# Kernel tuning notes

Hardware: AMD Instinct MI355X
Metric: run time of the kernel (lower is better)

## Reference

```python
import jax, jax.numpy as jnp
import numpy as np


def setup_inputs() -> dict:
    key = jax.random.key(0)
    ks = jax.random.split(key, 6)
    B, T, D, E, F = 2, 2048, 1024, 8, 2048
    x = jax.random.normal(ks[0], (B, T, D), dtype=jnp.float32)
    gate_w = jax.random.normal(ks[1], (D, E), dtype=jnp.float32) * (1.0 / np.sqrt(D))
    base_w1 = jax.random.normal(ks[2], (D, F), dtype=jnp.float32) * np.sqrt(2.0 / (D + F))
    base_w2 = jax.random.normal(ks[3], (F, D), dtype=jnp.float32) * np.sqrt(2.0 / (F + D))
    expert_w1 = base_w1[None] + jax.random.normal(ks[4], (E, D, F), dtype=jnp.float32) * 0.01
    expert_w2 = base_w2[None] + jax.random.normal(ks[5], (E, F, D), dtype=jnp.float32) * 0.01
    expert_b1 = jnp.zeros((E, F), dtype=jnp.float32)
    expert_b2 = jnp.zeros((E, D), dtype=jnp.float32)
    return {"x": x, "gate_w": gate_w, "expert_w1": expert_w1, "expert_b1": expert_b1,
            "expert_w2": expert_w2, "expert_b2": expert_b2}


def reference(x, gate_w, expert_w1, expert_b1, expert_w2, expert_b2):
    # Router (TopKRouter): top-2 routing with aux load-balance loss + z-loss
    E = gate_w.shape[-1]
    TOP_K = 2
    Z_LOSS_COEF = 1e-3
    logits = jnp.einsum('btd,de->bte', x, gate_w)                       # [B,T,E]
    top_vals, top_idx = jax.lax.top_k(logits, TOP_K)                    # [B,T,K]
    router_weights = jax.nn.softmax(top_vals, axis=-1)                  # [B,T,K]
    probs = jax.nn.softmax(logits, axis=-1)
    mask = jax.nn.one_hot(top_idx[..., 0], E, dtype=x.dtype)            # top-1 expert mask
    tokens_per_expert = mask.mean(axis=(0, 1))                          # [E]
    router_prob_per_expert = probs.mean(axis=(0, 1))                    # [E]
    aux_loss = E * jnp.sum(tokens_per_expert * router_prob_per_expert) \
               + jnp.mean(logits ** 2) * Z_LOSS_COEF

    # Expert FFNs: compute all experts densely, then gather top-k outputs.
    # (Same math as per-token weight gather, without the BTDF intermediate.)
    h = jnp.einsum('btd,edf->btef', x, expert_w1) + expert_b1           # [B,T,E,F]
    h = jax.nn.gelu(h, approximate=False)                               # torch F.gelu default = erf
    out_all = jnp.einsum('btef,efd->bted', h, expert_w2) + expert_b2    # [B,T,E,D]
    gathered = jnp.take_along_axis(out_all, top_idx[..., None], axis=2) # [B,T,K,D]
    output = jnp.einsum('btk,btkd->btd', router_weights, gathered)      # [B,T,D]
    return output, aux_loss
```

## Files before the change

kernel.cpp:

```cpp
#include <hip/hip_runtime.h>
#include <hip/hip_bf16.h>

#define NTOK 4096
#define DDIM 1024
#define NEXP 8
#define FDIM 2048
#define CAP  4096
#define RTOK 16
#define MT   16

typedef float f32x4 __attribute__((ext_vector_type(4)));
typedef short s16x8 __attribute__((ext_vector_type(8)));
typedef short s16x4 __attribute__((ext_vector_type(4)));

__device__ __forceinline__ unsigned short f2bf(float f) {
  unsigned int u = __float_as_uint(f);
  unsigned int r = u + 0x7fffu + ((u >> 16) & 1u);
  return (unsigned short)(r >> 16);
}

__device__ __forceinline__ void gload16(const void* g, void* l) {
  __builtin_amdgcn_global_load_lds(
      (__attribute__((address_space(1))) unsigned int*)(g),
      (__attribute__((address_space(3))) unsigned int*)(l), 16, 0, 0);
}

__global__ __launch_bounds__(256)
void k_transpose_cast(const float* __restrict__ src, unsigned short* __restrict__ dst,
                      int R, int C) {
  __shared__ float tile[64][68];
  const int e = blockIdx.z;
  const int c0 = blockIdx.x * 64, r0 = blockIdx.y * 64;
  const float* s = src + (size_t)e * R * C;
  unsigned short* d = dst + (size_t)e * R * C;
  const int tid = threadIdx.x;
  const int lr = tid >> 4, lc = (tid & 15) * 4;
  #pragma unroll
  for (int p = 0; p < 4; p++) {
    float4 v = *(const float4*)(s + (size_t)(r0 + p * 16 + lr) * C + c0 + lc);
    tile[p * 16 + lr][lc]     = v.x;
    tile[p * 16 + lr][lc + 1] = v.y;
    tile[p * 16 + lr][lc + 2] = v.z;
    tile[p * 16 + lr][lc + 3] = v.w;
  }
  __syncthreads();
  const int sc = tid >> 3, sr = (tid & 7) * 8;
  #pragma unroll
  for (int p = 0; p < 2; p++) {
    int c = p * 32 + sc;
    s16x8 o;
    #pragma unroll
    for (int j = 0; j < 8; j++) o[j] = (short)f2bf(tile[sr + j][c]);
    *(s16x8*)(d + (size_t)(c0 + c) * R + r0 + sr) = o;
  }
}

__global__ __launch_bounds__(128)
void k_router(const float* __restrict__ x, const float* __restrict__ gw,
              unsigned short* __restrict__ xb,
              float* __restrict__ topw, int* __restrict__ elist,
              int* __restrict__ ecnt, int* __restrict__ cnt1,
              float* __restrict__ psum, float* __restrict__ sqsum) {
  __shared__ float gwt[NEXP][DDIM + 4];
  __shared__ float xs[RTOK][264];
  __shared__ double lgd[RTOK][NEXP];
  __shared__ float bps[NEXP];
  __shared__ int bc[NEXP];
  __shared__ float bsq;
  const int tid = threadIdx.x;
  const int tok0 = blockIdx.x * RTOK;

  for (int i = tid; i < DDIM * NEXP; i += 128) {
    int d = i >> 3, e = i & 7;
    gwt[e][d] = gw[i];
  }
  if (tid < NEXP) { bps[tid] = 0.f; bc[tid] = 0; }
  if (tid == 0) bsq = 0.f;

  const int t = tid >> 3, e = tid & 7;
  double a0 = 0.0, a1 = 0.0, a2 = 0.0, a3 = 0.0;
  for (int c = 0; c < DDIM; c += 256) {
    __syncthreads();
    for (int i = tid; i < RTOK * 64; i += 128) {
      int r = i >> 6, c4 = i & 63;
      float4 v = *(const float4*)(x + (size_t)(tok0 + r) * DDIM + c + c4 * 4);
      *(float4*)&xs[r][c4 * 4] = v;
      s16x4 o;
      o[0] = (short)f2bf(v.x); o[1] = (short)f2bf(v.y);
      o[2] = (short)f2bf(v.z); o[3] = (short)f2bf(v.w);
      *(s16x4*)(xb + (size_t)(tok0 + r) * DDIM + c + c4 * 4) = o;
    }
    __syncthreads();
    #pragma unroll 8
    for (int d4 = 0; d4 < 64; d4++) {
      float4 xv = *(const float4*)&xs[t][d4 * 4];
      float4 gv = *(const float4*)&gwt[e][c + d4 * 4];
      a0 += (double)xv.x * (double)gv.x;
      a1 += (double)xv.y * (double)gv.y;
      a2 += (double)xv.z * (double)gv.z;
      a3 += (double)xv.w * (double)gv.w;
    }
  }
  lgd[t][e] = (a0 + a1) + (a2 + a3);
  __syncthreads();

  if (tid < RTOK) {
    int tok = tok0 + tid;
    double acc[NEXP];
    #pragma unroll
    for (int k = 0; k < NEXP; k++) acc[k] = lgd[tid][k];
    int i0 = 0; double v0 = acc[0];
    #pragma unroll
    for (int k = 1; k < NEXP; k++) if (acc[k] > v0) { v0 = acc[k]; i0 = k; }
    int i1 = (i0 == 0) ? 1 : 0; double v1 = acc[i1];
    #pragma unroll
    for (int k = 0; k < NEXP; k++) if (k != i0 && acc[k] > v1) { v1 = acc[k]; i1 = k; }
    float w0 = 1.0f / (1.0f + expf((float)(v1 - v0)));
    topw[2*tok] = w0; topw[2*tok + 1] = 1.0f - w0;
    int s0 = atomicAdd(&ecnt[i0], 1); elist[i0*CAP + s0] = 2*tok;
    int s1 = atomicAdd(&ecnt[i1], 1); elist[i1*CAP + s1] = 2*tok + 1;
    atomicAdd(&bc[i0], 1);
    float lm = (float)acc[0];
    #pragma unroll
    for (int k = 1; k < NEXP; k++) lm = fmaxf(lm, (float)acc[k]);
    float pe[NEXP], ps = 0.f, sq = 0.f;
    #pragma unroll
    for (int k = 0; k < NEXP; k++) {
      float le = (float)acc[k];
      pe[k] = expf(le - lm); ps += pe[k];
      sq += le * le;
    }
    float inv = 1.0f / ps;
    #pragma unroll
    for (int k = 0; k < NEXP; k++) atomicAdd(&bps[k], pe[k] * inv);
    atomicAdd(&bsq, sq);
  }
  __syncthreads();
  if (tid < NEXP) { atomicAdd(&psum[tid], bps[tid]); atomicAdd(&cnt1[tid], bc[tid]); }
  if (tid == 0) atomicAdd(sqsum, bsq);
}

template<int K, int N, bool GELU, bool ROWSHIFT>
__global__ __launch_bounds__(512)
void k_gemm(const unsigned short* __restrict__ A, const unsigned short* __restrict__ Bt,
            const float* __restrict__ bias, void* __restrict__ Out,
            const int* __restrict__ elist, const int* __restrict__ ecnt) {
  constexpr int BM = 128, BN = 128, BK = 128, WM = 2, WN = 4;
  constexpr int GX = N / BN;
  constexpr int TOT = GX * MT * NEXP;
  constexpr int CHUNK = TOT / 8;
  constexpr int AISS = BM / 32;
  constexpr int BISS = BN / 32;
  constexpr int MF = BM / WM / 16;
  constexpr int NF = BN / WN / 16;
  __shared__ unsigned char lsA[BM * 256];
  __shared__ unsigned char lsB[BN * 256];

  const int w = blockIdx.x;
  const int swz = (w & 7) * CHUNK + (w >> 3);
  const int e = swz / (GX * MT);
  const int loc = swz % (GX * MT);
  const int mt = loc % MT, nt = loc / MT;

  const int cnt = ecnt[e];
  const int m0 = mt * BM;
  if (m0 >= cnt) return;
  const int rv = min(BM, cnt - m0);
  const int* lst = elist + e * CAP + m0;
  const int tid = threadIdx.x, wv = tid >> 6, lane = tid & 63;
  const int wm = wv / WN, wn = wv % WN;
  const unsigned short* Be = Bt + (size_t)e * N * K;

  const unsigned short* agp[AISS];
  const unsigned short* bgp[BISS];
  int adst[AISS], bdst[BISS];
  const int cu = tid & 15;
  #pragma unroll
  for (int li = 0; li < AISS; li++) {
    int r = li * 32 + (tid >> 4);
    int rr = (r < rv) ? r : 0;
    int aid = lst[rr];
    int arow = ROWSHIFT ? (aid >> 1) : aid;
    int csrc = (cu ^ (r & 15)) * 16;
    agp[li] = A + (size_t)arow * K + (csrc >> 1);
    adst[li] = r * 256 + cu * 16;
  }
  #pragma unroll
  for (int li = 0; li < BISS; li++) {
    int r = li * 32 + (tid >> 4);
    int csrc = (cu ^ (r & 15)) * 16;
    bgp[li] = Be + (size_t)(nt * BN + r) * K + (csrc >> 1);
    bdst[li] = r * 256 + cu * 16;
  }

  f32x4 acc[MF][NF];
  #pragma unroll
  for (int mi = 0; mi < MF; mi++)
    #pragma unroll
    for (int ni = 0; ni < NF; ni++)
      acc[mi][ni] = (f32x4){0.f, 0.f, 0.f, 0.f};

  constexpr int NK = K / BK;
  for (int t = 0; t < NK; ++t) {
    const int k0 = t * BK;
    #pragma unroll
    for (int li = 0; li < AISS; li++) gload16(agp[li] + k0, &lsA[adst[li]]);
    #pragma unroll
    for (int li = 0; li < BISS; li++) gload16(bgp[li] + k0, &lsB[bdst[li]]);
    __syncthreads();
    #pragma unroll
    for (int ks = 0; ks < 4; ks++) {
      s16x8 af[MF], bf[NF];
      #pragma unroll
      for (int mi = 0; mi < MF; mi++) {
        int row = wm * (BM / WM) + mi * 16 + (lane & 15);
        int c16 = (ks * 4 + (lane >> 4)) ^ (row & 15);
        af[mi] = *(const s16x8*)&lsA[row * 256 + c16 * 16];
      }
      #pragma unroll
      for (int ni = 0; ni < NF; ni++) {
        int row = wn * (BN / WN) + ni * 16 + (lane & 15);
        int c16 = (ks * 4 + (lane >> 4)) ^ (row & 15);
        bf[ni] = *(const s16x8*)&lsB[row * 256 + c16 * 16];
      }
      #pragma unroll
      for (int mi = 0; mi < MF; mi++)
        #pragma unroll
        for (int ni = 0; ni < NF; ni++)
          acc[mi][ni] = __builtin_amdgcn_mfma_f32_16x16x32_bf16(af[mi], bf[ni], acc[mi][ni], 0, 0, 0);
    }
    __syncthreads();
  }

  const int g4 = (lane >> 4) * 4, cn = lane & 15;
  #pragma unroll
  for (int mi = 0; mi < MF; mi++) {
    #pragma unroll
    for (int reg = 0; reg < 4; reg++) {
      int r = wm * (BM / WM) + mi * 16 + g4 + reg;
      if (r < rv) {
        int aid = lst[r];
        #pragma unroll
        for (int ni = 0; ni < NF; ni++) {
          int n = nt * BN + wn * (BN / WN) + ni * 16 + cn;
          float v = acc[mi][ni][reg] + bias[(size_t)e * N + n];
          if constexpr (GELU) {
            v = 0.5f * v * (1.0f + erff(v * 0.70710678118654752f));
            ((unsigned short*)Out)[(size_t)aid * N + n] = f2bf(v);
          } else {
            ((float*)Out)[(size_t)aid * N + n] = v;
          }
        }
      }
    }
  }
}

__global__ void k_combine(const float* __restrict__ buf, const float* __restrict__ topw,
                          float* __restrict__ out) {
  int i = blockIdx.x * 256 + threadIdx.x;
  int t = i >> 8, c = i & 255;
  float w0 = topw[2*t], w1 = topw[2*t + 1];
  float4 a = ((const float4*)(buf + (size_t)(2*t) * DDIM))[c];
  float4 b = ((const float4*)(buf + (size_t)(2*t + 1) * DDIM))[c];
  float4 o;
  o.x = w0*a.x + w1*b.x; o.y = w0*a.y + w1*b.y;
  o.z = w0*a.z + w1*b.z; o.w = w0*a.w + w1*b.w;
  ((float4*)out)[i] = o;
}

__global__ void k_aux(const int* __restrict__ cnt1, const float* __restrict__ psum,
                      const float* __restrict__ sqsum, float* __restrict__ out) {
  if (threadIdx.x == 0 && blockIdx.x == 0) {
    float a = 0.f;
    for (int e = 0; e < NEXP; e++)
      a += ((float)cnt1[e] / (float)NTOK) * (psum[e] / (float)NTOK);
    out[(size_t)NTOK * DDIM] = (float)NEXP * a + (*sqsum) / (float)(NTOK * NEXP) * 1e-3f;
  }
}

extern "C" void kernel_launch(void* const* d_in, const int* in_sizes, int n_in,
                              void* d_out, int out_size, void* d_ws, size_t ws_size,
                              hipStream_t stream) {
  const float* x  = (const float*)d_in[0];
  const float* gw = (const float*)d_in[1];
  const float* w1 = (const float*)d_in[2];
  const float* b1 = (const float*)d_in[3];
  const float* w2 = (const float*)d_in[4];
  const float* b2 = (const float*)d_in[5];
  float* out = (float*)d_out;
  char* p = (char*)d_ws;

  int*   ecnt  = (int*)p;
  int*   cnt1  = (int*)(p + 32);
  float* psum  = (float*)(p + 64);
  float* sqsum = (float*)(p + 96);
  float* topw  = (float*)(p + 256);
  int*   elist = (int*)(p + 256 + 32768);
  unsigned short* xb  = (unsigned short*)(p + 256 + 32768 + 131072);
  unsigned short* w1t = xb  + (size_t)NTOK * DDIM;
  unsigned short* w2t = w1t + (size_t)NEXP * DDIM * FDIM;
  unsigned short* Hb  = w2t + (size_t)NEXP * DDIM * FDIM;
  float* obuf = (float*)(Hb + (size_t)NTOK * 2 * FDIM);

  hipMemsetAsync(p, 0, 128, stream);
  k_transpose_cast<<<dim3(FDIM/64, DDIM/64, NEXP), 256, 0, stream>>>(w1, w1t, DDIM, FDIM);
  k_transpose_cast<<<dim3(DDIM/64, FDIM/64, NEXP), 256, 0, stream>>>(w2, w2t, FDIM, DDIM);
  k_router<<<NTOK / RTOK, 128, 0, stream>>>(x, gw, xb, topw, elist, ecnt, cnt1, psum, sqsum);
  k_gemm<DDIM, FDIM, true,  true ><<<(FDIM/128)*MT*NEXP, 512, 0, stream>>>(xb, w1t, b1, Hb, elist, ecnt);
  k_gemm<FDIM, DDIM, false, false><<<(DDIM/128)*MT*NEXP, 512, 0, stream>>>(Hb, w2t, b2, obuf, elist, ecnt);
  k_combine<<<NTOK * DDIM / 4 / 256, 256, 0, stream>>>(obuf, topw, out);
  k_aux<<<1, 64, 0, stream>>>(cnt1, psum, sqsum, out);
}
```

Baseline: 251.6 us.

## Register-prefetch next K tile instead of direct global-to-LDS loads

Measured after the change: 261.2 us. +3.8%, slower.

```diff
diff --git a/kernel.cpp b/kernel.cpp
--- a/kernel.cpp
+++ b/kernel.cpp
@@ -19,10 +19,10 @@
   return (unsigned short)(r >> 16);
 }
 
-__device__ __forceinline__ void gload16(const void* g, void* l) {
-  __builtin_amdgcn_global_load_lds(
-      (__attribute__((address_space(1))) unsigned int*)(g),
-      (__attribute__((address_space(3))) unsigned int*)(l), 16, 0, 0);
+__device__ __forceinline__ void lgkm_barrier() {
+  asm volatile("s_waitcnt lgkmcnt(0)" ::: "memory");
+  __builtin_amdgcn_s_barrier();
+  __builtin_amdgcn_sched_barrier(0);
 }
 
 __global__ __launch_bounds__(256)
@@ -181,16 +181,14 @@
     int rr = (r < rv) ? r : 0;
     int aid = lst[rr];
     int arow = ROWSHIFT ? (aid >> 1) : aid;
-    int csrc = (cu ^ (r & 15)) * 16;
-    agp[li] = A + (size_t)arow * K + (csrc >> 1);
-    adst[li] = r * 256 + cu * 16;
+    agp[li] = A + (size_t)arow * K + cu * 8;
+    adst[li] = r * 256 + ((cu ^ (r & 15)) * 16);
   }
   #pragma unroll
   for (int li = 0; li < BISS; li++) {
     int r = li * 32 + (tid >> 4);
-    int csrc = (cu ^ (r & 15)) * 16;
-    bgp[li] = Be + (size_t)(nt * BN + r) * K + (csrc >> 1);
-    bdst[li] = r * 256 + cu * 16;
+    bgp[li] = Be + (size_t)(nt * BN + r) * K + cu * 8;
+    bdst[li] = r * 256 + ((cu ^ (r & 15)) * 16);
   }
 
   f32x4 acc[MF][NF];
@@ -201,13 +199,25 @@
       acc[mi][ni] = (f32x4){0.f, 0.f, 0.f, 0.f};
 
   constexpr int NK = K / BK;
+  s16x8 va[AISS], vb[BISS];
+  #pragma unroll
+  for (int li = 0; li < AISS; li++) va[li] = *(const s16x8*)(agp[li]);
+  #pragma unroll
+  for (int li = 0; li < BISS; li++) vb[li] = *(const s16x8*)(bgp[li]);
+
   for (int t = 0; t < NK; ++t) {
-    const int k0 = t * BK;
-    #pragma unroll
-    for (int li = 0; li < AISS; li++) gload16(agp[li] + k0, &lsA[adst[li]]);
-    #pragma unroll
-    for (int li = 0; li < BISS; li++) gload16(bgp[li] + k0, &lsB[bdst[li]]);
-    __syncthreads();
+    #pragma unroll
+    for (int li = 0; li < AISS; li++) *(s16x8*)&lsA[adst[li]] = va[li];
+    #pragma unroll
+    for (int li = 0; li < BISS; li++) *(s16x8*)&lsB[bdst[li]] = vb[li];
+    if (t + 1 < NK) {
+      const int k1 = (t + 1) * BK;
+      #pragma unroll
+      for (int li = 0; li < AISS; li++) va[li] = *(const s16x8*)(agp[li] + k1);
+      #pragma unroll
+      for (int li = 0; li < BISS; li++) vb[li] = *(const s16x8*)(bgp[li] + k1);
+    }
+    lgkm_barrier();
     #pragma unroll
     for (int ks = 0; ks < 4; ks++) {
       s16x8 af[MF], bf[NF];
@@ -229,7 +239,7 @@
         for (int ni = 0; ni < NF; ni++)
           acc[mi][ni] = __builtin_amdgcn_mfma_f32_16x16x32_bf16(af[mi], bf[ni], acc[mi][ni], 0, 0, 0);
     }
-    __syncthreads();
+    lgkm_barrier();
   }
 
   const int g4 = (lane >> 4) * 4, cn = lane & 15;
```

## Fuse weight transposes and router into one prep kernel; fold aux into combine

Applied to the files above, without the earlier changes.

Result: no change. 249.2 us (-0.9%).

```diff
diff --git a/kernel.cpp b/kernel.cpp
--- a/kernel.cpp
+++ b/kernel.cpp
@@ -6,7 +6,7 @@
 #define NEXP 8
 #define FDIM 2048
 #define CAP  4096
-#define RTOK 16
+#define RTOK 32
 #define MT   16
 
 typedef float f32x4 __attribute__((ext_vector_type(4)));
@@ -25,15 +25,13 @@
       (__attribute__((address_space(3))) unsigned int*)(l), 16, 0, 0);
 }
 
-__global__ __launch_bounds__(256)
-void k_transpose_cast(const float* __restrict__ src, unsigned short* __restrict__ dst,
-                      int R, int C) {
-  __shared__ float tile[64][68];
-  const int e = blockIdx.z;
-  const int c0 = blockIdx.x * 64, r0 = blockIdx.y * 64;
+__device__ __forceinline__ void transpose_tile(const float* __restrict__ src,
+                                               unsigned short* __restrict__ dst,
+                                               int R, int C, int c0, int r0, int e,
+                                               char* smem, int tid) {
+  float (*tile)[68] = (float(*)[68])smem;
   const float* s = src + (size_t)e * R * C;
   unsigned short* d = dst + (size_t)e * R * C;
-  const int tid = threadIdx.x;
   const int lr = tid >> 4, lc = (tid & 15) * 4;
   #pragma unroll
   for (int p = 0; p < 4; p++) {
@@ -55,33 +53,49 @@
   }
 }
 
-__global__ __launch_bounds__(128)
-void k_router(const float* __restrict__ x, const float* __restrict__ gw,
-              unsigned short* __restrict__ xb,
-              float* __restrict__ topw, int* __restrict__ elist,
-              int* __restrict__ ecnt, int* __restrict__ cnt1,
-              float* __restrict__ psum, float* __restrict__ sqsum) {
-  __shared__ float gwt[NEXP][DDIM + 4];
-  __shared__ float xs[RTOK][264];
-  __shared__ double lgd[RTOK][NEXP];
-  __shared__ float bps[NEXP];
-  __shared__ int bc[NEXP];
-  __shared__ float bsq;
-  const int tid = threadIdx.x;
-  const int tok0 = blockIdx.x * RTOK;
-
-  for (int i = tid; i < DDIM * NEXP; i += 128) {
+__global__ __launch_bounds__(256)
+void k_prep(const float* __restrict__ x, const float* __restrict__ gw,
+            const float* __restrict__ w1, const float* __restrict__ w2,
+            unsigned short* __restrict__ xb, unsigned short* __restrict__ w1t,
+            unsigned short* __restrict__ w2t,
+            float* __restrict__ topw, int* __restrict__ elist,
+            int* __restrict__ ecnt, int* __restrict__ cnt1,
+            float* __restrict__ psum, float* __restrict__ sqsum) {
+  __shared__ char smem[68864];
+  const int bid = blockIdx.x, tid = threadIdx.x;
+
+  if (bid < 4096) {
+    int cx = bid & 31, ry = (bid >> 5) & 15, e = bid >> 9;
+    transpose_tile(w1, w1t, DDIM, FDIM, cx * 64, ry * 64, e, smem, tid);
+    return;
+  }
+  if (bid < 8192) {
+    int b = bid - 4096;
+    int cx = b & 15, ry = (b >> 4) & 31, e = b >> 9;
+    transpose_tile(w2, w2t, FDIM, DDIM, cx * 64, ry * 64, e, smem, tid);
+    return;
+  }
+
+  float (*gwt)[DDIM + 4] = (float(*)[DDIM + 4])smem;
+  float (*xs)[264]       = (float(*)[264])(smem + 32896);
+  double (*lgd)[NEXP]    = (double(*)[NEXP])(smem + 66688);
+  float* bps = (float*)(smem + 68736);
+  int*   bc  = (int*)(smem + 68768);
+  float* bsq = (float*)(smem + 68800);
+  const int tok0 = (bid - 8192) * RTOK;
+
+  for (int i = tid; i < DDIM * NEXP; i += 256) {
     int d = i >> 3, e = i & 7;
     gwt[e][d] = gw[i];
   }
   if (tid < NEXP) { bps[tid] = 0.f; bc[tid] = 0; }
-  if (tid == 0) bsq = 0.f;
+  if (tid == 0) *bsq = 0.f;
 
   const int t = tid >> 3, e = tid & 7;
   double a0 = 0.0, a1 = 0.0, a2 = 0.0, a3 = 0.0;
   for (int c = 0; c < DDIM; c += 256) {
     __syncthreads();
-    for (int i = tid; i < RTOK * 64; i += 128) {
+    for (int i = tid; i < RTOK * 64; i += 256) {
       int r = i >> 6, c4 = i & 63;
       float4 v = *(const float4*)(x + (size_t)(tok0 + r) * DDIM + c + c4 * 4);
       *(float4*)&xs[r][c4 * 4] = v;
@@ -133,11 +147,11 @@
     float inv = 1.0f / ps;
     #pragma unroll
     for (int k = 0; k < NEXP; k++) atomicAdd(&bps[k], pe[k] * inv);
-    atomicAdd(&bsq, sq);
+    atomicAdd(bsq, sq);
   }
   __syncthreads();
   if (tid < NEXP) { atomicAdd(&psum[tid], bps[tid]); atomicAdd(&cnt1[tid], bc[tid]); }
-  if (tid == 0) atomicAdd(sqsum, bsq);
+  if (tid == 0) atomicAdd(sqsum, *bsq);
 }
 
 template<int K, int N, bool GELU, bool ROWSHIFT>
@@ -257,7 +271,9 @@
 }
 
 __global__ void k_combine(const float* __restrict__ buf, const float* __restrict__ topw,
-                          float* __restrict__ out) {
+                          float* __restrict__ out,
+                          const int* __restrict__ cnt1, const float* __restrict__ psum,
+                          const float* __restrict__ sqsum) {
   int i = blockIdx.x * 256 + threadIdx.x;
   int t = i >> 8, c = i & 255;
   float w0 = topw[2*t], w1 = topw[2*t + 1];
@@ -267,15 +283,11 @@
   o.x = w0*a.x + w1*b.x; o.y = w0*a.y + w1*b.y;
   o.z = w0*a.z + w1*b.z; o.w = w0*a.w + w1*b.w;
   ((float4*)out)[i] = o;
-}
-
-__global__ void k_aux(const int* __restrict__ cnt1, const float* __restrict__ psum,
-                      const float* __restrict__ sqsum, float* __restrict__ out) {
-  if (threadIdx.x == 0 && blockIdx.x == 0) {
-    float a = 0.f;
+  if (i == 0) {
+    float s = 0.f;
     for (int e = 0; e < NEXP; e++)
-      a += ((float)cnt1[e] / (float)NTOK) * (psum[e] / (float)NTOK);
-    out[(size_t)NTOK * DDIM] = (float)NEXP * a + (*sqsum) / (float)(NTOK * NEXP) * 1e-3f;
+      s += ((float)cnt1[e] / (float)NTOK) * (psum[e] / (float)NTOK);
+    out[(size_t)NTOK * DDIM] = (float)NEXP * s + (*sqsum) / (float)(NTOK * NEXP) * 1e-3f;
   }
 }
 
@@ -304,11 +316,9 @@
   float* obuf = (float*)(Hb + (size_t)NTOK * 2 * FDIM);
 
   hipMemsetAsync(p, 0, 128, stream);
-  k_transpose_cast<<<dim3(FDIM/64, DDIM/64, NEXP), 256, 0, stream>>>(w1, w1t, DDIM, FDIM);
-  k_transpose_cast<<<dim3(DDIM/64, FDIM/64, NEXP), 256, 0, stream>>>(w2, w2t, FDIM, DDIM);
-  k_router<<<NTOK / RTOK, 128, 0, stream>>>(x, gw, xb, topw, elist, ecnt, cnt1, psum, sqsum);
+  k_prep<<<8192 + NTOK / RTOK, 256, 0, stream>>>(x, gw, w1, w2, xb, w1t, w2t,
+                                                 topw, elist, ecnt, cnt1, psum, sqsum);
   k_gemm<DDIM, FDIM, true,  true ><<<(FDIM/128)*MT*NEXP, 512, 0, stream>>>(xb, w1t, b1, Hb, elist, ecnt);
   k_gemm<FDIM, DDIM, false, false><<<(DDIM/128)*MT*NEXP, 512, 0, stream>>>(Hb, w2t, b2, obuf, elist, ecnt);
-  k_combine<<<NTOK * DDIM / 4 / 256, 256, 0, stream>>>(obuf, topw, out);
-  k_aux<<<1, 64, 0, stream>>>(cnt1, psum, sqsum, out);
-}
+  k_combine<<<NTOK * DDIM / 4 / 256, 256, 0, stream>>>(obuf, topw, out, cnt1, psum, sqsum);
+}
```
